# Performance work log

Hardware: AMD Instinct MI355X
Metric: run time of the kernel (lower is better)

The kernel has to match this reference:

```python
import jax, jax.numpy as jnp
import numpy as np

NUM_NODES = 100000
NUM_REL = 8
HIDDEN = 128
NUM_EDGES = 1600000
NUM_LAYERS = 2


def setup_inputs() -> dict:
    key = jax.random.key(0)
    k1, k2, k3, k4, k5 = jax.random.split(key, 5)
    x = jnp.arange(NUM_NODES, dtype=jnp.int64)
    edge_index = jax.random.randint(k1, (2, NUM_EDGES), 0, NUM_NODES, dtype=jnp.int64)
    edge_type = jax.random.randint(k2, (NUM_EDGES,), 0, NUM_REL, dtype=jnp.int64)
    emb = jax.random.normal(k3, (NUM_NODES, HIDDEN), dtype=jnp.float32) * 0.1
    W = jax.random.normal(k4, (NUM_LAYERS, NUM_REL, HIDDEN, HIDDEN), dtype=jnp.float32) * (1.0 / np.sqrt(HIDDEN))
    root = jax.random.normal(k5, (NUM_LAYERS, HIDDEN, HIDDEN), dtype=jnp.float32) * (1.0 / np.sqrt(HIDDEN))
    bias = jnp.zeros((NUM_LAYERS, HIDDEN), dtype=jnp.float32)
    return {"x": x, "edge_index": edge_index, "edge_type": edge_type,
            "emb": emb, "W": W, "root": root, "bias": bias}


def _rgcn_conv(h, src, dst, etype, W_l, root_l, bias_l):
    # h: [N, d]; W_l: [R, d, d]
    n = h.shape[0]
    r = W_l.shape[0]
    # Transform all nodes by every relation weight: [R, N, d]
    xW = jnp.einsum('nd,rdf->rnf', h, W_l)
    # Per-edge message gathered by (relation, source): [E, d]
    msg = xW[etype, src]
    # Mean-normalize per (target node, relation), matching PyG aggr='mean'
    seg = dst * r + etype  # combined (node, relation) segment id
    cnt = jax.ops.segment_sum(jnp.ones(msg.shape[0], dtype=h.dtype), seg,
                              num_segments=n * r)
    norm = 1.0 / jnp.maximum(cnt[seg], 1.0)
    agg = jax.ops.segment_sum(msg * norm[:, None], dst, num_segments=n)
    return agg + h @ root_l + bias_l


def reference(x, edge_index, edge_type, emb, W, root, bias):
    src, dst = edge_index[0], edge_index[1]
    h = emb[x]  # embedding lookup
    for l in range(NUM_LAYERS):
        h = _rgcn_conv(h, src, dst, edge_type, W[l], root[l], bias[l])
        h = jax.nn.relu(h)
    return h
```

## Files before the change

### kernel.cpp

```cpp
#include <hip/hip_runtime.h>

typedef unsigned int u32;
typedef unsigned short u16;
typedef __attribute__((ext_vector_type(8))) short short8;
typedef __attribute__((ext_vector_type(4))) float f32x4;

#define DD 128
#define RREL 8
#define KCAT 1152
#define NKT 9
#define SCAN_CHUNK 4096

static __device__ __forceinline__ u16 f2bf(float f) {
  u32 u = __builtin_bit_cast(u32, f);
  u32 r = (u + 0x7fffu + ((u >> 16) & 1u)) >> 16;
  return (u16)r;
}
static __device__ __forceinline__ float bflo(u32 v) { return __builtin_bit_cast(float, v << 16); }
static __device__ __forceinline__ float bfhi(u32 v) { return __builtin_bit_cast(float, v & 0xffff0000u); }

__global__ __launch_bounds__(256) void k_convw(const float* __restrict__ W,
                                               const float* __restrict__ root,
                                               uint4* __restrict__ wt) {
  int t = blockIdx.x * 256 + threadIdx.x;
  if (t >= 2 * NKT * 2048) return;
  int l = t / (NKT * 2048);
  int rem = t - l * (NKT * 2048);
  int kt = rem >> 11;
  int pos = rem & 2047;
  int col = pos >> 4;
  int cbx = pos & 15;
  int cb = cbx ^ (col & 7);
  int k0 = kt * DD + cb * 8;
  u16 vals[8];
#pragma unroll
  for (int i = 0; i < 8; ++i) {
    int k = k0 + i;
    float v;
    if (k < DD) {
      v = root[(size_t)l * DD * DD + k * DD + col];
    } else {
      int km = k - DD;
      v = W[((size_t)l * RREL + (km >> 7)) * DD * DD + (size_t)(km & 127) * DD + col];
    }
    vals[i] = f2bf(v);
  }
  wt[t] = *(uint4*)vals;
}

__global__ __launch_bounds__(256) void k_gather(const int* __restrict__ x,
                                                const float* __restrict__ emb,
                                                u16* __restrict__ acat, int N) {
  int t = blockIdx.x * 256 + threadIdx.x;
  if (t >= N * 16) return;
  int node = t >> 4, part = t & 15;
  const float4* e4 = (const float4*)(emb + (size_t)x[node] * DD + part * 8);
  float4 f0 = e4[0], f1 = e4[1];
  uint4 u;
  u.x = (u32)f2bf(f0.x) | ((u32)f2bf(f0.y) << 16);
  u.y = (u32)f2bf(f0.z) | ((u32)f2bf(f0.w) << 16);
  u.z = (u32)f2bf(f1.x) | ((u32)f2bf(f1.y) << 16);
  u.w = (u32)f2bf(f1.z) | ((u32)f2bf(f1.w) << 16);
  *(uint4*)(acat + (size_t)node * KCAT + part * 8) = u;
}

__global__ __launch_bounds__(256) void k_hist(const int* __restrict__ ei,
                                              const int* __restrict__ et,
                                              int* __restrict__ cnt, int E) {
  int base = (blockIdx.x * 256 + threadIdx.x) * 8;
  if (base + 7 < E) {
    int4 dA = *(const int4*)(ei + E + base);
    int4 dB = *(const int4*)(ei + E + base + 4);
    int4 tA = *(const int4*)(et + base);
    int4 tB = *(const int4*)(et + base + 4);
    atomicAdd(&cnt[dA.x * 8 + tA.x], 1);
    atomicAdd(&cnt[dA.y * 8 + tA.y], 1);
    atomicAdd(&cnt[dA.z * 8 + tA.z], 1);
    atomicAdd(&cnt[dA.w * 8 + tA.w], 1);
    atomicAdd(&cnt[dB.x * 8 + tB.x], 1);
    atomicAdd(&cnt[dB.y * 8 + tB.y], 1);
    atomicAdd(&cnt[dB.z * 8 + tB.z], 1);
    atomicAdd(&cnt[dB.w * 8 + tB.w], 1);
  } else {
    for (int e = base; e < E; ++e) atomicAdd(&cnt[ei[E + e] * 8 + et[e]], 1);
  }
}

__global__ __launch_bounds__(256) void k_scan_reduce(const int* __restrict__ cnt,
                                                     int* __restrict__ blksum, int nseg) {
  __shared__ int s[256];
  int b = blockIdx.x, t = threadIdx.x;
  int base = b * SCAN_CHUNK;
  int sum = 0;
  for (int i = 0; i < 16; ++i) {
    int idx = base + i * 256 + t;
    if (idx < nseg) sum += cnt[idx];
  }
  s[t] = sum;
  __syncthreads();
  for (int st = 128; st > 0; st >>= 1) {
    if (t < st) s[t] += s[t + st];
    __syncthreads();
  }
  if (t == 0) blksum[b] = s[0];
}

__global__ void k_scan_top(int* __restrict__ blksum, int nblk, int* __restrict__ off,
                           int nseg, int E) {
  if (threadIdx.x == 0 && blockIdx.x == 0) {
    int run = 0;
    for (int b = 0; b < nblk; ++b) { int v = blksum[b]; blksum[b] = run; run += v; }
    off[nseg] = E;
  }
}

__global__ __launch_bounds__(256) void k_scan_write(const int* __restrict__ cnt,
                                                    const int* __restrict__ blksum,
                                                    int* __restrict__ off, int nseg) {
  __shared__ int s[256];
  int b = blockIdx.x, t = threadIdx.x;
  int base = b * SCAN_CHUNK + t * 16;
  int v[16];
  int sum = 0;
#pragma unroll
  for (int i = 0; i < 16; ++i) {
    int idx = base + i;
    v[i] = (idx < nseg) ? cnt[idx] : 0;
    sum += v[i];
  }
  s[t] = sum;
  __syncthreads();
  for (int st = 1; st < 256; st <<= 1) {
    int add = (t >= st) ? s[t - st] : 0;
    __syncthreads();
    s[t] += add;
    __syncthreads();
  }
  int run = blksum[b] + s[t] - sum;
#pragma unroll
  for (int i = 0; i < 16; ++i) {
    int idx = base + i;
    if (idx < nseg) off[idx] = run;
    run += v[i];
  }
}

__global__ __launch_bounds__(256) void k_scatter(const int* __restrict__ ei,
                                                 const int* __restrict__ et,
                                                 int* __restrict__ fill,
                                                 int* __restrict__ sorted, int E) {
  int base = (blockIdx.x * 256 + threadIdx.x) * 8;
  if (base + 7 < E) {
    int4 sA = *(const int4*)(ei + base);
    int4 sB = *(const int4*)(ei + base + 4);
    int4 dA = *(const int4*)(ei + E + base);
    int4 dB = *(const int4*)(ei + E + base + 4);
    int4 tA = *(const int4*)(et + base);
    int4 tB = *(const int4*)(et + base + 4);
    int p0 = atomicAdd(&fill[dA.x * 8 + tA.x], 1);
    int p1 = atomicAdd(&fill[dA.y * 8 + tA.y], 1);
    int p2 = atomicAdd(&fill[dA.z * 8 + tA.z], 1);
    int p3 = atomicAdd(&fill[dA.w * 8 + tA.w], 1);
    int p4 = atomicAdd(&fill[dB.x * 8 + tB.x], 1);
    int p5 = atomicAdd(&fill[dB.y * 8 + tB.y], 1);
    int p6 = atomicAdd(&fill[dB.z * 8 + tB.z], 1);
    int p7 = atomicAdd(&fill[dB.w * 8 + tB.w], 1);
    sorted[p0] = sA.x;
    sorted[p1] = sA.y;
    sorted[p2] = sA.z;
    sorted[p3] = sA.w;
    sorted[p4] = sB.x;
    sorted[p5] = sB.y;
    sorted[p6] = sB.z;
    sorted[p7] = sB.w;
  } else {
    for (int e = base; e < E; ++e) {
      int pos = atomicAdd(&fill[ei[E + e] * 8 + et[e]], 1);
      sorted[pos] = ei[e];
    }
  }
}

static __device__ __forceinline__ void add8(float* a, uint4 v) {
  a[0] += bflo(v.x); a[1] += bfhi(v.x);
  a[2] += bflo(v.y); a[3] += bfhi(v.y);
  a[4] += bflo(v.z); a[5] += bfhi(v.z);
  a[6] += bflo(v.w); a[7] += bfhi(v.w);
}

__global__ __launch_bounds__(256) void k_agg(const int* __restrict__ off,
                                             const int* __restrict__ sorted,
                                             u16* acat, int N, int E) {
  int wave = threadIdx.x >> 6, lane = threadIdx.x & 63;
  int grp = lane >> 3, oct = lane & 7;
  int dst = blockIdx.x * 32 + wave * 8 + grp;
  if (dst >= N) return;
  int4 b0 = *(const int4*)(off + dst * 8);
  int4 b1 = *(const int4*)(off + dst * 8 + 4);
  int je = off[dst * 8 + 8];
  int cs = b0.x;
  int e1 = b0.y, e2 = b0.z, e3 = b0.w, e4 = b1.x, e5 = b1.y, e6 = b1.z, e7 = b1.w, e8 = je;
  u16* ambase = acat + (size_t)dst * KCAT + DD + oct * 16;
  float a[16];
#pragma unroll
  for (int i = 0; i < 16; ++i) a[i] = 0.f;
  int j = cs;
  int r = 0;
  int lastidx = (E > 0) ? E - 1 : 0;
  while (true) {
    while (r < 8 && j >= e1) {
      int cnt = e1 - cs;
      float norm = (cnt > 0) ? 1.0f / (float)cnt : 0.f;
      uint4 w0, w1;
      w0.x = (u32)f2bf(a[0] * norm) | ((u32)f2bf(a[1] * norm) << 16);
      w0.y = (u32)f2bf(a[2] * norm) | ((u32)f2bf(a[3] * norm) << 16);
      w0.z = (u32)f2bf(a[4] * norm) | ((u32)f2bf(a[5] * norm) << 16);
      w0.w = (u32)f2bf(a[6] * norm) | ((u32)f2bf(a[7] * norm) << 16);
      w1.x = (u32)f2bf(a[8] * norm) | ((u32)f2bf(a[9] * norm) << 16);
      w1.y = (u32)f2bf(a[10] * norm) | ((u32)f2bf(a[11] * norm) << 16);
      w1.z = (u32)f2bf(a[12] * norm) | ((u32)f2bf(a[13] * norm) << 16);
      w1.w = (u32)f2bf(a[14] * norm) | ((u32)f2bf(a[15] * norm) << 16);
      uint4* outp = (uint4*)(ambase + (size_t)r * DD);
      outp[0] = w0;
      outp[1] = w1;
#pragma unroll
      for (int i = 0; i < 16; ++i) a[i] = 0.f;
      cs = e1;
      e1 = e2; e2 = e3; e3 = e4; e4 = e5; e5 = e6; e6 = e7; e7 = e8;
      ++r;
    }
    if (r >= 8) break;
    int j1 = j + 1;
    bool two = (j1 < e1);
    int s0 = sorted[j];
    int s1 = sorted[two ? j1 : lastidx];
    const uint4* p0 = (const uint4*)(acat + (size_t)s0 * KCAT + oct * 16);
    const uint4* p1 = (const uint4*)(acat + (size_t)s1 * KCAT + oct * 16);
    uint4 v0 = p0[0], v0b = p0[1];
    uint4 v1 = p1[0], v1b = p1[1];
    if (!two) {
      v1.x = v1.y = v1.z = v1.w = 0u;
      v1b.x = v1b.y = v1b.z = v1b.w = 0u;
    }
    add8(a, v0); add8(a + 8, v0b);
    add8(a, v1); add8(a + 8, v1b);
    j += two ? 2 : 1;
  }
}

template <bool LAST>
__global__ __launch_bounds__(512) void k_gemm(u16* acat, const uint4* __restrict__ wt,
                                              const float* __restrict__ bias,
                                              float* __restrict__ dout, int M) {
  __shared__ uint4 ldsB[2][2048];
  int tid = threadIdx.x, wave = tid >> 6, lane = tid & 63;
  int rowbase = blockIdx.x * 128 + wave * 16;
  int arow = rowbase + (lane & 15);
  int arc = arow < M ? arow : M - 1;
  int klane = (lane >> 4) << 3;
  f32x4 acc[8];
#pragma unroll
  for (int c = 0; c < 8; ++c) acc[c] = (f32x4)0.f;

#define STAGE(KT, BUF)                                                                   \
  do {                                                                                   \
    const uint4* gsrc = wt + (size_t)(KT) * 2048;                                        \
    _Pragma("unroll") for (int i_ = 0; i_ < 4; ++i_) {                                   \
      int cid_ = i_ * 512 + tid;                                                         \
      __builtin_amdgcn_global_load_lds(                                                  \
          (const __attribute__((address_space(1))) uint4*)(gsrc + cid_),                 \
          (__attribute__((address_space(3))) uint4*)&ldsB[BUF][cid_], 16, 0, 0);         \
    }                                                                                    \
  } while (0)

  STAGE(0, 0);
  for (int kt = 0; kt < NKT; ++kt) {
    int cur = kt & 1;
    __syncthreads();
    if (kt + 1 < NKT) STAGE(kt + 1, cur ^ 1);
#pragma unroll
    for (int kc = 0; kc < 4; ++kc) {
      short8 a = *(const short8*)(acat + (size_t)arc * KCAT + kt * DD + kc * 32 + klane);
      int chunk = kc * 4 + (lane >> 4);
#pragma unroll
      for (int c = 0; c < 8; ++c) {
        int col = c * 16 + (lane & 15);
        const short8* bp = (const short8*)&ldsB[cur][col * 16 + (chunk ^ (col & 7))];
        acc[c] = __builtin_amdgcn_mfma_f32_16x16x32_bf16(a, *bp, acc[c], 0, 0, 0);
      }
    }
  }
#undef STAGE

  int crow0 = rowbase + ((lane >> 4) << 2);
  int ccol = lane & 15;
#pragma unroll
  for (int c = 0; c < 8; ++c) {
    int col = c * 16 + ccol;
    float bv = bias[col];
#pragma unroll
    for (int i = 0; i < 4; ++i) {
      int row = crow0 + i;
      if (row < M) {
        float v = fmaxf(acc[c][i] + bv, 0.f);
        if (LAST) dout[(size_t)row * DD + col] = v;
        else acat[(size_t)row * KCAT + col] = f2bf(v);
      }
    }
  }
}

extern "C" void kernel_launch(void* const* d_in, const int* in_sizes, int n_in,
                              void* d_out, int out_size, void* d_ws, size_t ws_size,
                              hipStream_t stream) {
  const int* x = (const int*)d_in[0];
  const int* ei = (const int*)d_in[1];
  const int* et = (const int*)d_in[2];
  const float* emb = (const float*)d_in[3];
  const float* W = (const float*)d_in[4];
  const float* root = (const float*)d_in[5];
  const float* bias = (const float*)d_in[6];

  const int N = in_sizes[0];
  const int E = in_sizes[2];
  const int NSEG = N * RREL;

  size_t o = 0;
  auto al = [&](size_t b) { size_t r = o; o = (o + b + 255) & ~(size_t)255; return r; };
  size_t off_o = al(((size_t)NSEG + 1) * 4);
  size_t cnt_o = al((size_t)NSEG * 4);
  size_t fill_o = al((size_t)NSEG * 4);
  size_t sorted_o = al((size_t)E * 4);
  size_t blk_o = al(4096);
  size_t wt_o = al((size_t)2 * NKT * 2048 * 16);
  size_t acat_o = al((size_t)N * KCAT * 2);
  (void)acat_o;

  char* ws = (char*)d_ws;
  int* off = (int*)(ws + off_o);
  int* cnt = (int*)(ws + cnt_o);
  int* fill = (int*)(ws + fill_o);
  int* sorted = (int*)(ws + sorted_o);
  int* blks = (int*)(ws + blk_o);
  uint4* wt = (uint4*)(ws + wt_o);
  u16* acat = (u16*)(ws + acat_o);
  float* outf = (float*)d_out;

  k_convw<<<(2 * NKT * 2048 + 255) / 256, 256, 0, stream>>>(W, root, wt);
  k_gather<<<(N * 16 + 255) / 256, 256, 0, stream>>>(x, emb, acat, N);
  hipMemsetAsync(cnt, 0, (size_t)NSEG * 4, stream);
  int egrid = ((E + 7) / 8 + 255) / 256;
  k_hist<<<egrid, 256, 0, stream>>>(ei, et, cnt, E);
  int nblk = (NSEG + SCAN_CHUNK - 1) / SCAN_CHUNK;
  k_scan_reduce<<<nblk, 256, 0, stream>>>(cnt, blks, NSEG);
  k_scan_top<<<1, 64, 0, stream>>>(blks, nblk, off, NSEG, E);
  k_scan_write<<<nblk, 256, 0, stream>>>(cnt, blks, off, NSEG);
  hipMemcpyAsync(fill, off, (size_t)NSEG * 4, hipMemcpyDeviceToDevice, stream);
  k_scatter<<<egrid, 256, 0, stream>>>(ei, et, fill, sorted, E);

  int gx = (N + 127) / 128;
  int agrid = (N + 31) / 32;
  k_agg<<<agrid, 256, 0, stream>>>(off, sorted, acat, N, E);
  k_gemm<false><<<gx, 512, 0, stream>>>(acat, wt, bias, nullptr, N);
  k_agg<<<agrid, 256, 0, stream>>>(off, sorted, acat, N, E);
  k_gemm<true><<<gx, 512, 0, stream>>>(acat, wt + (size_t)NKT * 2048, bias + DD, outf, N);
}
```

Before: 554.5 us.

## Pre-swizzle weights for direct MFMA loads, shard scatter by destination, fuse fill copy

The weight conversion kernel now writes B in the exact per-lane MFMA fragment order. The GEMM can then read B directly from global memory or cache, with no LDS staging or barriers, and it runs with 64-row, 256-thread blocks. The scatter kernel is split into 8 destination shards per edge chunk to improve atomic and write locality. It re-reads the edge arrays 8 times in exchange. The fill copy is folded into the scan-write kernel, and the histogram uses 4 edges per thread.

```diff
diff --git a/kernel.cpp b/kernel.cpp
--- a/kernel.cpp
+++ b/kernel.cpp
@@ -10,6 +10,8 @@
 #define KCAT 1152
 #define NKT 9
 #define SCAN_CHUNK 4096
+#define SC_EPT 8
+#define SC_CHUNK (256 * SC_EPT)
 
 static __device__ __forceinline__ u16 f2bf(float f) {
   u32 u = __builtin_bit_cast(u32, f);
@@ -21,17 +23,19 @@
 
 __global__ __launch_bounds__(256) void k_convw(const float* __restrict__ W,
                                                const float* __restrict__ root,
-                                               uint4* __restrict__ wt) {
+                                               uint4* __restrict__ wt2) {
   int t = blockIdx.x * 256 + threadIdx.x;
   if (t >= 2 * NKT * 2048) return;
   int l = t / (NKT * 2048);
   int rem = t - l * (NKT * 2048);
   int kt = rem >> 11;
-  int pos = rem & 2047;
-  int col = pos >> 4;
-  int cbx = pos & 15;
-  int cb = cbx ^ (col & 7);
-  int k0 = kt * DD + cb * 8;
+  int rem2 = rem & 2047;
+  int c = rem2 >> 8;
+  int kc = (rem2 >> 6) & 3;
+  int lane = rem2 & 63;
+  int p = lane & 15, q = lane >> 4;
+  int col = c * 16 + p;
+  int k0 = kt * DD + kc * 32 + q * 8;
   u16 vals[8];
 #pragma unroll
   for (int i = 0; i < 8; ++i) {
@@ -45,7 +49,7 @@
     }
     vals[i] = f2bf(v);
   }
-  wt[t] = *(uint4*)vals;
+  wt2[t] = *(uint4*)vals;
 }
 
 __global__ __launch_bounds__(256) void k_gather(const int* __restrict__ x,
@@ -67,20 +71,14 @@
 __global__ __launch_bounds__(256) void k_hist(const int* __restrict__ ei,
                                               const int* __restrict__ et,
                                               int* __restrict__ cnt, int E) {
-  int base = (blockIdx.x * 256 + threadIdx.x) * 8;
-  if (base + 7 < E) {
-    int4 dA = *(const int4*)(ei + E + base);
-    int4 dB = *(const int4*)(ei + E + base + 4);
-    int4 tA = *(const int4*)(et + base);
-    int4 tB = *(const int4*)(et + base + 4);
-    atomicAdd(&cnt[dA.x * 8 + tA.x], 1);
-    atomicAdd(&cnt[dA.y * 8 + tA.y], 1);
-    atomicAdd(&cnt[dA.z * 8 + tA.z], 1);
-    atomicAdd(&cnt[dA.w * 8 + tA.w], 1);
-    atomicAdd(&cnt[dB.x * 8 + tB.x], 1);
-    atomicAdd(&cnt[dB.y * 8 + tB.y], 1);
-    atomicAdd(&cnt[dB.z * 8 + tB.z], 1);
-    atomicAdd(&cnt[dB.w * 8 + tB.w], 1);
+  int base = (blockIdx.x * 256 + threadIdx.x) * 4;
+  if (base + 3 < E) {
+    int4 d4 = *(const int4*)(ei + E + base);
+    int4 t4 = *(const int4*)(et + base);
+    atomicAdd(&cnt[d4.x * 8 + t4.x], 1);
+    atomicAdd(&cnt[d4.y * 8 + t4.y], 1);
+    atomicAdd(&cnt[d4.z * 8 + t4.z], 1);
+    atomicAdd(&cnt[d4.w * 8 + t4.w], 1);
   } else {
     for (int e = base; e < E; ++e) atomicAdd(&cnt[ei[E + e] * 8 + et[e]], 1);
   }
@@ -116,7 +114,8 @@
 
 __global__ __launch_bounds__(256) void k_scan_write(const int* __restrict__ cnt,
                                                     const int* __restrict__ blksum,
-                                                    int* __restrict__ off, int nseg) {
+                                                    int* __restrict__ off,
+                                                    int* __restrict__ fill, int nseg) {
   __shared__ int s[256];
   int b = blockIdx.x, t = threadIdx.x;
   int base = b * SCAN_CHUNK + t * 16;
@@ -140,7 +139,7 @@
 #pragma unroll
   for (int i = 0; i < 16; ++i) {
     int idx = base + i;
-    if (idx < nseg) off[idx] = run;
+    if (idx < nseg) { off[idx] = run; fill[idx] = run; }
     run += v[i];
   }
 }
@@ -148,35 +147,35 @@
 __global__ __launch_bounds__(256) void k_scatter(const int* __restrict__ ei,
                                                  const int* __restrict__ et,
                                                  int* __restrict__ fill,
-                                                 int* __restrict__ sorted, int E) {
-  int base = (blockIdx.x * 256 + threadIdx.x) * 8;
-  if (base + 7 < E) {
+                                                 int* __restrict__ sorted, int E, int N8) {
+  int shard = blockIdx.x & 7;
+  int chunk = blockIdx.x >> 3;
+  int base = chunk * SC_CHUNK + threadIdx.x * SC_EPT;
+  int lo = shard * N8, hi = lo + N8;
+  if (base + SC_EPT <= E) {
     int4 sA = *(const int4*)(ei + base);
     int4 sB = *(const int4*)(ei + base + 4);
     int4 dA = *(const int4*)(ei + E + base);
     int4 dB = *(const int4*)(ei + E + base + 4);
     int4 tA = *(const int4*)(et + base);
     int4 tB = *(const int4*)(et + base + 4);
-    int p0 = atomicAdd(&fill[dA.x * 8 + tA.x], 1);
-    int p1 = atomicAdd(&fill[dA.y * 8 + tA.y], 1);
-    int p2 = atomicAdd(&fill[dA.z * 8 + tA.z], 1);
-    int p3 = atomicAdd(&fill[dA.w * 8 + tA.w], 1);
-    int p4 = atomicAdd(&fill[dB.x * 8 + tB.x], 1);
-    int p5 = atomicAdd(&fill[dB.y * 8 + tB.y], 1);
-    int p6 = atomicAdd(&fill[dB.z * 8 + tB.z], 1);
-    int p7 = atomicAdd(&fill[dB.w * 8 + tB.w], 1);
-    sorted[p0] = sA.x;
-    sorted[p1] = sA.y;
-    sorted[p2] = sA.z;
-    sorted[p3] = sA.w;
-    sorted[p4] = sB.x;
-    sorted[p5] = sB.y;
-    sorted[p6] = sB.z;
-    sorted[p7] = sB.w;
+    int sv[8] = {sA.x, sA.y, sA.z, sA.w, sB.x, sB.y, sB.z, sB.w};
+    int dv[8] = {dA.x, dA.y, dA.z, dA.w, dB.x, dB.y, dB.z, dB.w};
+    int tv[8] = {tA.x, tA.y, tA.z, tA.w, tB.x, tB.y, tB.z, tB.w};
+#pragma unroll
+    for (int i = 0; i < 8; ++i) {
+      if (dv[i] >= lo && dv[i] < hi) {
+        int pos = atomicAdd(&fill[dv[i] * 8 + tv[i]], 1);
+        sorted[pos] = sv[i];
+      }
+    }
   } else {
-    for (int e = base; e < E; ++e) {
-      int pos = atomicAdd(&fill[ei[E + e] * 8 + et[e]], 1);
-      sorted[pos] = ei[e];
+    for (int e = base; e < E && e < base + SC_EPT; ++e) {
+      int dd = ei[E + e];
+      if (dd >= lo && dd < hi) {
+        int pos = atomicAdd(&fill[dd * 8 + et[e]], 1);
+        sorted[pos] = ei[e];
+      }
     }
   }
 }
@@ -249,54 +248,38 @@
 }
 
 template <bool LAST>
-__global__ __launch_bounds__(512) void k_gemm(u16* acat, const uint4* __restrict__ wt,
+__global__ __launch_bounds__(256) void k_gemm(u16* acat, const uint4* __restrict__ wt2,
                                               const float* __restrict__ bias,
                                               float* __restrict__ dout, int M) {
-  __shared__ uint4 ldsB[2][2048];
   int tid = threadIdx.x, wave = tid >> 6, lane = tid & 63;
-  int rowbase = blockIdx.x * 128 + wave * 16;
-  int arow = rowbase + (lane & 15);
+  int p = lane & 15, q = lane >> 4;
+  int rowbase = blockIdx.x * 64 + wave * 16;
+  int arow = rowbase + p;
   int arc = arow < M ? arow : M - 1;
-  int klane = (lane >> 4) << 3;
+  const u16* arp = acat + (size_t)arc * KCAT + q * 8;
+  const uint4* bp = wt2 + lane;
   f32x4 acc[8];
 #pragma unroll
   for (int c = 0; c < 8; ++c) acc[c] = (f32x4)0.f;
-
-#define STAGE(KT, BUF)                                                                   \
-  do {                                                                                   \
-    const uint4* gsrc = wt + (size_t)(KT) * 2048;                                        \
-    _Pragma("unroll") for (int i_ = 0; i_ < 4; ++i_) {                                   \
-      int cid_ = i_ * 512 + tid;                                                         \
-      __builtin_amdgcn_global_load_lds(                                                  \
-          (const __attribute__((address_space(1))) uint4*)(gsrc + cid_),                 \
-          (__attribute__((address_space(3))) uint4*)&ldsB[BUF][cid_], 16, 0, 0);         \
-    }                                                                                    \
-  } while (0)
-
-  STAGE(0, 0);
+#pragma unroll
   for (int kt = 0; kt < NKT; ++kt) {
-    int cur = kt & 1;
-    __syncthreads();
-    if (kt + 1 < NKT) STAGE(kt + 1, cur ^ 1);
+    short8 a[4];
+#pragma unroll
+    for (int kc = 0; kc < 4; ++kc)
+      a[kc] = *(const short8*)(arp + kt * DD + kc * 32);
 #pragma unroll
     for (int kc = 0; kc < 4; ++kc) {
-      short8 a = *(const short8*)(acat + (size_t)arc * KCAT + kt * DD + kc * 32 + klane);
-      int chunk = kc * 4 + (lane >> 4);
 #pragma unroll
       for (int c = 0; c < 8; ++c) {
-        int col = c * 16 + (lane & 15);
-        const short8* bp = (const short8*)&ldsB[cur][col * 16 + (chunk ^ (col & 7))];
-        acc[c] = __builtin_amdgcn_mfma_f32_16x16x32_bf16(a, *bp, acc[c], 0, 0, 0);
+        const short8* b = (const short8*)(bp + ((size_t)((kt * 8 + c) * 4 + kc)) * 64);
+        acc[c] = __builtin_amdgcn_mfma_f32_16x16x32_bf16(a[kc], *b, acc[c], 0, 0, 0);
       }
     }
   }
-#undef STAGE
-
-  int crow0 = rowbase + ((lane >> 4) << 2);
-  int ccol = lane & 15;
+  int crow0 = rowbase + (q << 2);
 #pragma unroll
   for (int c = 0; c < 8; ++c) {
-    int col = c * 16 + ccol;
+    int col = c * 16 + p;
     float bv = bias[col];
 #pragma unroll
     for (int i = 0; i < 4; ++i) {
@@ -342,26 +325,26 @@
   int* fill = (int*)(ws + fill_o);
   int* sorted = (int*)(ws + sorted_o);
   int* blks = (int*)(ws + blk_o);
-  uint4* wt = (uint4*)(ws + wt_o);
+  uint4* wt2 = (uint4*)(ws + wt_o);
   u16* acat = (u16*)(ws + acat_o);
   float* outf = (float*)d_out;
 
-  k_convw<<<(2 * NKT * 2048 + 255) / 256, 256, 0, stream>>>(W, root, wt);
+  k_convw<<<(2 * NKT * 2048 + 255) / 256, 256, 0, stream>>>(W, root, wt2);
   k_gather<<<(N * 16 + 255) / 256, 256, 0, stream>>>(x, emb, acat, N);
   hipMemsetAsync(cnt, 0, (size_t)NSEG * 4, stream);
-  int egrid = ((E + 7) / 8 + 255) / 256;
-  k_hist<<<egrid, 256, 0, stream>>>(ei, et, cnt, E);
+  k_hist<<<((E + 3) / 4 + 255) / 256, 256, 0, stream>>>(ei, et, cnt, E);
   int nblk = (NSEG + SCAN_CHUNK - 1) / SCAN_CHUNK;
   k_scan_reduce<<<nblk, 256, 0, stream>>>(cnt, blks, NSEG);
   k_scan_top<<<1, 64, 0, stream>>>(blks, nblk, off, NSEG, E);
-  k_scan_write<<<nblk, 256, 0, stream>>>(cnt, blks, off, NSEG);
-  hipMemcpyAsync(fill, off, (size_t)NSEG * 4, hipMemcpyDeviceToDevice, stream);
-  k_scatter<<<egrid, 256, 0, stream>>>(ei, et, fill, sorted, E);
-
-  int gx = (N + 127) / 128;
+  k_scan_write<<<nblk, 256, 0, stream>>>(cnt, blks, off, fill, NSEG);
+  int N8 = (N + 7) / 8;
+  int nch = (E + SC_CHUNK - 1) / SC_CHUNK;
+  k_scatter<<<nch * 8, 256, 0, stream>>>(ei, et, fill, sorted, E, N8);
+
+  int gx = (N + 63) / 64;
   int agrid = (N + 31) / 32;
   k_agg<<<agrid, 256, 0, stream>>>(off, sorted, acat, N, E);
-  k_gemm<false><<<gx, 512, 0, stream>>>(acat, wt, bias, nullptr, N);
+  k_gemm<false><<<gx, 256, 0, stream>>>(acat, wt2, bias, nullptr, N);
   k_agg<<<agrid, 256, 0, stream>>>(off, sorted, acat, N, E);
-  k_gemm<true><<<gx, 512, 0, stream>>>(acat, wt + (size_t)NKT * 2048, bias + DD, outf, N);
-}
+  k_gemm<true><<<gx, 256, 0, stream>>>(acat, wt2 + (size_t)NKT * 2048, bias + DD, outf, N);
+}
```

Result: slower. 612.0 us (+10.4%).
